# Performance work log

Measured on AMD Instinct MI355X. Metric: run time of the kernel, lower is better.

Reference implementation:

```python
import jax, jax.numpy as jnp
import numpy as np

C = 128
HEADS = 4
GROUPS = 16
EPS = 1e-5


def setup_inputs() -> dict:
    key = jax.random.key(0)
    ks = jax.random.split(key, 4)
    x = jax.random.normal(ks[0], (2, C, 16, 16, 16), dtype=jnp.float32)
    gn_w = jnp.ones((C,), dtype=jnp.float32)
    gn_b = jnp.zeros((C,), dtype=jnp.float32)
    w_qkv = jax.random.normal(ks[1], (3 * C, C), dtype=jnp.float32) * (1.0 / np.sqrt(C))
    w_out = jax.random.normal(ks[2], (C, C), dtype=jnp.float32) * (1.0 / np.sqrt(C))
    b_out = jnp.zeros((C,), dtype=jnp.float32)
    return {"x": x, "gn_w": gn_w, "gn_b": gn_b, "w_qkv": w_qkv, "w_out": w_out, "b_out": b_out}


def reference(x, gn_w, gn_b, w_qkv, w_out, b_out):
    b, c, d, h, w = x.shape
    L = d * h * w
    xf = x.reshape(b, c, L)  # flatten spatial dims -> tokens

    # GroupNorm over (channels-in-group, spatial)
    xg = xf.reshape(b, GROUPS, c // GROUPS * L)
    mean = jnp.mean(xg, axis=-1, keepdims=True)
    var = jnp.var(xg, axis=-1, keepdims=True)
    xn = ((xg - mean) * jax.lax.rsqrt(var + EPS)).reshape(b, c, L)
    xn = xn * gn_w[None, :, None] + gn_b[None, :, None]

    # 1x1 conv QKV projection (no bias)
    qkv = jnp.einsum('bcl,oc->bol', xn, w_qkv)  # (b, 3c, L)
    q, k, v = jnp.split(qkv, 3, axis=1)
    dh = c // HEADS
    q = q.reshape(b, HEADS, dh, L).transpose(0, 1, 3, 2)  # (b,H,L,dh)
    k = k.reshape(b, HEADS, dh, L)                        # (b,H,dh,L)
    v = v.reshape(b, HEADS, dh, L).transpose(0, 1, 3, 2)  # (b,H,L,dh)

    scale = dh ** (-0.5)
    attn = jnp.einsum('bhld,bhdm->bhlm', q, k) * scale    # (b,H,L,L)
    attn = jax.nn.softmax(attn, axis=-1)
    o = jnp.einsum('bhlm,bhmd->bhld', attn, v)            # (b,H,L,dh)
    o = o.transpose(0, 1, 3, 2).reshape(b, c, L)

    # output 1x1 conv with bias
    o = jnp.einsum('bcl,oc->bol', o, w_out) + b_out[None, :, None]
    return x + o.reshape(b, c, d, h, w)
```

## Files before the change

### kernel.cpp

```cpp
#include <hip/hip_runtime.h>
#include <math.h>

#define BB 2
#define CCH 128
#define LL 4096
#define HEADS 4
#define DH 32
#define EPSV 1e-5f
#define NSP 4

typedef float f32x4 __attribute__((ext_vector_type(4)));
typedef short bf16x8 __attribute__((ext_vector_type(8)));

__device__ inline unsigned short f2bf(float x) {
    union { float f; unsigned u; } v; v.f = x;
    unsigned r = v.u + 0x7fffu + ((v.u >> 16) & 1u);
    return (unsigned short)(r >> 16);
}
__device__ inline float bfbits2f(unsigned bits_hi16) {
    union { unsigned u; float f; } v; v.u = bits_hi16; return v.f;
}
__device__ inline float bfu(unsigned short s) {
    union { unsigned u; float f; } v; v.u = (unsigned)s << 16; return v.f;
}
__device__ inline unsigned cvtpk(float lo, float hi) {
    unsigned r;
    asm("v_cvt_pk_bf16_f32 %0, %1, %2" : "=v"(r) : "v"(lo), "v"(hi));
    return r;
}

__global__ __launch_bounds__(256) void gn_part(const float* __restrict__ x,
                                               float* __restrict__ ps, float* __restrict__ ps2) {
    const float* xp = x + (size_t)blockIdx.x * 4096;
    float s = 0.f, s2 = 0.f;
#pragma unroll
    for (int it = 0; it < 4; ++it) {
        float4 v = *(const float4*)(xp + it * 1024 + threadIdx.x * 4);
        s += v.x + v.y + v.z + v.w;
        s2 += v.x * v.x + v.y * v.y + v.z * v.z + v.w * v.w;
    }
    for (int off = 32; off; off >>= 1) {
        s += __shfl_down(s, off);
        s2 += __shfl_down(s2, off);
    }
    __shared__ float rs[4], rs2[4];
    int wave = threadIdx.x >> 6, lane = threadIdx.x & 63;
    if (lane == 0) { rs[wave] = s; rs2[wave] = s2; }
    __syncthreads();
    if (threadIdx.x == 0) {
        ps[blockIdx.x] = rs[0] + rs[1] + rs[2] + rs[3];
        ps2[blockIdx.x] = rs2[0] + rs2[1] + rs2[2] + rs2[3];
    }
}

__global__ void gn_final(const float* __restrict__ ps, const float* __restrict__ ps2,
                         float* __restrict__ sm, float* __restrict__ sr) {
    int t = threadIdx.x;
    if (t >= 32) return;
    float s = 0.f, s2 = 0.f;
#pragma unroll
    for (int i = 0; i < 8; ++i) { s += ps[t * 8 + i]; s2 += ps2[t * 8 + i]; }
    float mean = s / 32768.f;
    float var = s2 / 32768.f - mean * mean;
    sm[t] = mean;
    sr[t] = rsqrtf(var + EPSV);
}

__global__ __launch_bounds__(256) void prep_w(const float* __restrict__ w_qkv,
                                              const float* __restrict__ w_out,
                                              unsigned short* __restrict__ Wqh, unsigned short* __restrict__ Wql,
                                              unsigned short* __restrict__ Woh, unsigned short* __restrict__ Wol) {
    int i = blockIdx.x * 256 + threadIdx.x;
    const float qscale = 0.2550350f;
    if (i < 49152) {
        float v = w_qkv[i];
        if (i < 16384) v *= qscale;
        unsigned short h = f2bf(v);
        Wqh[i] = h;
        Wql[i] = f2bf(v - bfbits2f((unsigned)h << 16));
    } else {
        int j = i - 49152;
        float v = w_out[j];
        unsigned short h = f2bf(v);
        Woh[j] = h;
        Wol[j] = f2bf(v - bfbits2f((unsigned)h << 16));
    }
}

__global__ __launch_bounds__(256) void gn_apply_t(const float* __restrict__ x,
                                                  const float* __restrict__ gw, const float* __restrict__ gb,
                                                  const float* __restrict__ sm, const float* __restrict__ sr,
                                                  unsigned short* __restrict__ xth, unsigned short* __restrict__ xtl) {
    int lt = blockIdx.x, ct = blockIdx.y, b = blockIdx.z;
    int c0 = ct * 32, l0 = lt * 64;
    __shared__ float wsh[32], bsh[32], msh[4], rsh[4];
    __shared__ unsigned short sh[32][72], sl[32][72];
    if (threadIdx.x < 32) { wsh[threadIdx.x] = gw[c0 + threadIdx.x]; bsh[threadIdx.x] = gb[c0 + threadIdx.x]; }
    if (threadIdx.x < 4) {
        int g = (c0 >> 3) + threadIdx.x;
        msh[threadIdx.x] = sm[b * 16 + g];
        rsh[threadIdx.x] = sr[b * 16 + g];
    }
    __syncthreads();
#pragma unroll
    for (int it = 0; it < 2; ++it) {
        int idx = it * 256 + threadIdx.x;
        int cc = idx >> 4, l4 = idx & 15;
        float4 v = *(const float4*)(x + ((size_t)(b * CCH + c0 + cc)) * LL + l0 + l4 * 4);
        float mn = msh[cc >> 3], rstd = rsh[cc >> 3], w = wsh[cc], bv = bsh[cc];
        float a0 = (v.x - mn) * rstd * w + bv;
        float a1 = (v.y - mn) * rstd * w + bv;
        float a2 = (v.z - mn) * rstd * w + bv;
        float a3 = (v.w - mn) * rstd * w + bv;
        unsigned uh01 = cvtpk(a0, a1), uh23 = cvtpk(a2, a3);
        float r0 = a0 - bfbits2f(uh01 << 16), r1 = a1 - bfbits2f(uh01 & 0xffff0000u);
        float r2 = a2 - bfbits2f(uh23 << 16), r3 = a3 - bfbits2f(uh23 & 0xffff0000u);
        unsigned ul01 = cvtpk(r0, r1), ul23 = cvtpk(r2, r3);
        *(uint2*)&sh[cc][l4 * 4] = make_uint2(uh01, uh23);
        *(uint2*)&sl[cc][l4 * 4] = make_uint2(ul01, ul23);
    }
    __syncthreads();
    int l = threadIdx.x >> 2, c8 = threadIdx.x & 3;
    unsigned hw[4], lw[4];
#pragma unroll
    for (int j = 0; j < 4; ++j) {
        int c = c8 * 8 + 2 * j;
        hw[j] = (unsigned)sh[c][l] | ((unsigned)sh[c + 1][l] << 16);
        lw[j] = (unsigned)sl[c][l] | ((unsigned)sl[c + 1][l] << 16);
    }
    *(uint4*)(xth + ((size_t)b * LL + l0 + l) * CCH + c0 + c8 * 8) = make_uint4(hw[0], hw[1], hw[2], hw[3]);
    *(uint4*)(xtl + ((size_t)b * LL + l0 + l) * CCH + c0 + c8 * 8) = make_uint4(lw[0], lw[1], lw[2], lw[3]);
}

__global__ __launch_bounds__(64) void qkv_gemm(const unsigned short* __restrict__ xth,
                                               const unsigned short* __restrict__ xtl,
                                               const unsigned short* __restrict__ Wqh,
                                               const unsigned short* __restrict__ Wql,
                                               unsigned short* __restrict__ Qd,
                                               unsigned short* __restrict__ Kd,
                                               unsigned short* __restrict__ Vb) {
    int lt = blockIdx.x, og = blockIdx.y, b = blockIdx.z;
    int lane = threadIdx.x & 63, lm = lane & 15, lg = lane >> 4;
    int l0 = lt * 16;
    bf16x8 ah[4], al[4];
#pragma unroll
    for (int ks = 0; ks < 4; ++ks) {
        size_t off = ((size_t)b * LL + l0 + lm) * CCH + ks * 32 + 8 * lg;
        ah[ks] = *(const bf16x8*)(xth + off);
        al[ks] = *(const bf16x8*)(xtl + off);
    }
    f32x4 acc[8];
#pragma unroll
    for (int ot = 0; ot < 8; ++ot) acc[ot] = (f32x4){0.f, 0.f, 0.f, 0.f};
#pragma unroll
    for (int ot = 0; ot < 8; ++ot) {
#pragma unroll
        for (int ks = 0; ks < 4; ++ks) {
            size_t woff = (size_t)((og * 8 + ot) * 16 + lm) * CCH + ks * 32 + 8 * lg;
            bf16x8 wh = *(const bf16x8*)(Wqh + woff);
            bf16x8 wl = *(const bf16x8*)(Wql + woff);
            acc[ot] = __builtin_amdgcn_mfma_f32_16x16x32_bf16(ah[ks], wh, acc[ot], 0, 0, 0);
            acc[ot] = __builtin_amdgcn_mfma_f32_16x16x32_bf16(ah[ks], wl, acc[ot], 0, 0, 0);
            acc[ot] = __builtin_amdgcn_mfma_f32_16x16x32_bf16(al[ks], wh, acc[ot], 0, 0, 0);
        }
    }
    unsigned short* base = (og == 0) ? Qd : (og == 1) ? Kd : Vb;
#pragma unroll
    for (int ot = 0; ot < 8; ++ot) {
        int h = ot >> 1, d = (ot & 1) * 16 + lm;
        uint2 u;
        u.x = cvtpk(acc[ot][0], acc[ot][1]);
        u.y = cvtpk(acc[ot][2], acc[ot][3]);
        *(uint2*)(base + ((size_t)(b * HEADS + h) * DH + d) * LL + l0 + 4 * lg) = u;
    }
}

__global__ __launch_bounds__(256) void trQK(const unsigned short* __restrict__ Qd,
                                            const unsigned short* __restrict__ Kd,
                                            unsigned short* __restrict__ Qb,
                                            unsigned short* __restrict__ Kb) {
    int lt = blockIdx.x, bh = blockIdx.y, sel = blockIdx.z;
    const unsigned short* src = sel ? Kd : Qd;
    unsigned short* dst = sel ? Kb : Qb;
    int l0 = lt * 256;
    __shared__ unsigned short st[32][264];
#pragma unroll
    for (int it = 0; it < 4; ++it) {
        int idx = it * 256 + threadIdx.x;
        int d = idx >> 5, l8 = idx & 31;
        uint4 v = *(const uint4*)(src + ((size_t)bh * DH + d) * LL + l0 + l8 * 8);
        *(uint4*)&st[d][l8 * 8] = v;
    }
    __syncthreads();
    int t = threadIdx.x;
    unsigned w[16];
#pragma unroll
    for (int dp = 0; dp < 16; ++dp)
        w[dp] = (unsigned)st[2 * dp][t] | ((unsigned)st[2 * dp + 1][t] << 16);
    uint4* dp4 = (uint4*)(dst + ((size_t)bh * LL + l0 + t) * DH);
#pragma unroll
    for (int i = 0; i < 4; ++i)
        dp4[i] = make_uint4(w[4 * i], w[4 * i + 1], w[4 * i + 2], w[4 * i + 3]);
}

__global__ __launch_bounds__(256) void attn_kernel(const unsigned short* __restrict__ Qp,
                                                   const unsigned short* __restrict__ Kp,
                                                   const unsigned short* __restrict__ Vp,
                                                   unsigned short* __restrict__ AccB, float* __restrict__ Ls) {
    __shared__ __align__(16) unsigned short Ksh[2][64][40];
    __shared__ __align__(16) unsigned short Vsh[2][32][72];
    __shared__ __align__(16) short Pl[4][2][16][72];
    int id = blockIdx.x;
    int combo = id & 31, qb = id >> 5;
    int bh = combo >> 2, sp = combo & 3;
    int wid = threadIdx.x >> 6, lane = threadIdx.x & 63, lm = lane & 15, lg = lane >> 4;
    int q0 = qb * 128 + wid * 32;
    int kv0 = sp * 1024;
    int t = threadIdx.x;

    const unsigned short* Kbh = Kp + (size_t)bh * LL * DH;
    const unsigned short* Vbh = Vp + (size_t)bh * DH * LL;

    bf16x8 qf[2];
    qf[0] = *(const bf16x8*)(Qp + ((size_t)bh * LL + q0 + lm) * DH + 8 * lg);
    qf[1] = *(const bf16x8*)(Qp + ((size_t)bh * LL + q0 + 16 + lm) * DH + 8 * lg);

    f32x4 accO[2][2];
#pragma unroll
    for (int qi = 0; qi < 2; ++qi)
#pragma unroll
        for (int dt = 0; dt < 2; ++dt) accO[qi][dt] = (f32x4){0.f, 0.f, 0.f, 0.f};
    float plsum[2] = {0.f, 0.f};
    const f32x4 cbias = {-24.f, -24.f, -24.f, -24.f};

    int skv = t >> 2, ssl = (t & 3) * 8;
    int svd = t >> 3, svs = (t & 7) * 8;
    const uint4* gK = (const uint4*)(Kbh + (size_t)(kv0 + skv) * DH + ssl);
    const uint4* gV = (const uint4*)(Vbh + (size_t)svd * LL + kv0 + svs);
    uint4 kreg = *gK;
    uint4 vreg = *gV;

    for (int tt = 0; tt < 16; ++tt) {
        int cur = tt & 1;
        *(uint4*)&Ksh[cur][skv][ssl] = kreg;
        *(uint4*)&Vsh[cur][svd][svs] = vreg;
        if (tt < 15) { gK += 256; gV += 8; kreg = *gK; vreg = *gV; }
        __syncthreads();

        bf16x8 kf[4];
#pragma unroll
        for (int kc = 0; kc < 4; ++kc)
            kf[kc] = *(const bf16x8*)&Ksh[cur][kc * 16 + lm][lg * 8];
        f32x4 s[2][4];
#pragma unroll
        for (int qi = 0; qi < 2; ++qi)
#pragma unroll
            for (int kc = 0; kc < 4; ++kc)
                s[qi][kc] = __builtin_amdgcn_mfma_f32_16x16x32_bf16(kf[kc], qf[qi], cbias, 0, 0, 0);

        bf16x8 vf[2][2];
#pragma unroll
        for (int ch = 0; ch < 2; ++ch)
#pragma unroll
            for (int dt = 0; dt < 2; ++dt)
                vf[ch][dt] = *(const bf16x8*)&Vsh[cur][dt * 16 + lm][ch * 32 + 8 * lg];

#pragma unroll
        for (int qi = 0; qi < 2; ++qi) {
#pragma unroll
            for (int kc = 0; kc < 4; ++kc) {
                float e0 = __builtin_amdgcn_exp2f(s[qi][kc][0]);
                float e1 = __builtin_amdgcn_exp2f(s[qi][kc][1]);
                float e2 = __builtin_amdgcn_exp2f(s[qi][kc][2]);
                float e3 = __builtin_amdgcn_exp2f(s[qi][kc][3]);
                plsum[qi] += (e0 + e1) + (e2 + e3);
                uint2 u;
                u.x = cvtpk(e0, e1);
                u.y = cvtpk(e2, e3);
                *(uint2*)&Pl[wid][qi][lm][kc * 16 + 4 * lg] = u;
            }
            bf16x8 pf[2];
#pragma unroll
            for (int ch = 0; ch < 2; ++ch)
                pf[ch] = *(const bf16x8*)&Pl[wid][qi][lm][ch * 32 + 8 * lg];
#pragma unroll
            for (int ch = 0; ch < 2; ++ch)
#pragma unroll
                for (int dt = 0; dt < 2; ++dt)
                    accO[qi][dt] = __builtin_amdgcn_mfma_f32_16x16x32_bf16(vf[ch][dt], pf[ch], accO[qi][dt], 0, 0, 0);
        }
    }

#pragma unroll
    for (int qi = 0; qi < 2; ++qi) {
        float pl = plsum[qi];
        pl += __shfl_xor(pl, 16);
        pl += __shfl_xor(pl, 32);
#pragma unroll
        for (int dt = 0; dt < 2; ++dt) {
            uint2 u;
            u.x = cvtpk(accO[qi][dt][0], accO[qi][dt][1]);
            u.y = cvtpk(accO[qi][dt][2], accO[qi][dt][3]);
            *(uint2*)(AccB + ((size_t)(sp * 8 + bh) * LL + q0 + qi * 16 + lm) * DH + dt * 16 + 4 * lg) = u;
        }
        if (lg == 0) Ls[(size_t)(sp * 8 + bh) * LL + q0 + qi * 16 + lm] = pl;
    }
}

__global__ __launch_bounds__(256) void out_gemm(const unsigned short* __restrict__ AccB,
                                                const float* __restrict__ Ls,
                                                const unsigned short* __restrict__ Woh,
                                                const unsigned short* __restrict__ Wol,
                                                const float* __restrict__ bo,
                                                const float* __restrict__ x,
                                                float* __restrict__ out) {
    int lt = blockIdx.x, b = blockIdx.y;
    int wid = threadIdx.x >> 6, lane = threadIdx.x & 63, lm = lane & 15, lg = lane >> 4;
    int l0 = lt * 16;
    bf16x8 af[4];
#pragma unroll
    for (int ks = 0; ks < 4; ++ks) {
        int bh = b * HEADS + ks;
        float sum[8];
#pragma unroll
        for (int j = 0; j < 8; ++j) sum[j] = 0.f;
        float ls = 0.f;
#pragma unroll
        for (int sp = 0; sp < NSP; ++sp) {
            const unsigned short* ap = AccB + ((size_t)(sp * 8 + bh) * LL + l0 + lm) * DH + 8 * lg;
            uint4 v = *(const uint4*)ap;
            unsigned w0 = v.x, w1 = v.y, w2 = v.z, w3 = v.w;
            sum[0] += bfu((unsigned short)w0); sum[1] += bfu((unsigned short)(w0 >> 16));
            sum[2] += bfu((unsigned short)w1); sum[3] += bfu((unsigned short)(w1 >> 16));
            sum[4] += bfu((unsigned short)w2); sum[5] += bfu((unsigned short)(w2 >> 16));
            sum[6] += bfu((unsigned short)w3); sum[7] += bfu((unsigned short)(w3 >> 16));
            ls += Ls[(size_t)(sp * 8 + bh) * LL + l0 + lm];
        }
        float inv = 1.f / ls;
        union { unsigned u[4]; bf16x8 v; } cv;
        cv.u[0] = cvtpk(sum[0] * inv, sum[1] * inv);
        cv.u[1] = cvtpk(sum[2] * inv, sum[3] * inv);
        cv.u[2] = cvtpk(sum[4] * inv, sum[5] * inv);
        cv.u[3] = cvtpk(sum[6] * inv, sum[7] * inv);
        af[ks] = cv.v;
    }
    f32x4 acc[2];
    acc[0] = (f32x4){0.f, 0.f, 0.f, 0.f};
    acc[1] = (f32x4){0.f, 0.f, 0.f, 0.f};
#pragma unroll
    for (int oi = 0; oi < 2; ++oi) {
        int ot = wid * 2 + oi;
#pragma unroll
        for (int ks = 0; ks < 4; ++ks) {
            size_t woff = (size_t)(ot * 16 + lm) * CCH + ks * 32 + 8 * lg;
            bf16x8 wh = *(const bf16x8*)(Woh + woff);
            bf16x8 wl = *(const bf16x8*)(Wol + woff);
            acc[oi] = __builtin_amdgcn_mfma_f32_16x16x32_bf16(af[ks], wh, acc[oi], 0, 0, 0);
            acc[oi] = __builtin_amdgcn_mfma_f32_16x16x32_bf16(af[ks], wl, acc[oi], 0, 0, 0);
        }
    }
#pragma unroll
    for (int oi = 0; oi < 2; ++oi) {
        int oc = (wid * 2 + oi) * 16 + lm;
        float bias = bo[oc];
        size_t off = ((size_t)b * CCH + oc) * LL + l0 + 4 * lg;
        f32x4 xr = *(const f32x4*)(x + off);
        f32x4 r = acc[oi];
        r[0] += bias + xr[0];
        r[1] += bias + xr[1];
        r[2] += bias + xr[2];
        r[3] += bias + xr[3];
        *(f32x4*)(out + off) = r;
    }
}

extern "C" void kernel_launch(void* const* d_in, const int* in_sizes, int n_in,
                              void* d_out, int out_size, void* d_ws, size_t ws_size,
                              hipStream_t stream) {
    const float* x = (const float*)d_in[0];
    const float* gn_w = (const float*)d_in[1];
    const float* gn_b = (const float*)d_in[2];
    const float* w_qkv = (const float*)d_in[3];
    const float* w_out = (const float*)d_in[4];
    const float* b_out = (const float*)d_in[5];
    float* out = (float*)d_out;

    char* W = (char*)d_ws;
    unsigned short* xth = (unsigned short*)(W);
    unsigned short* xtl = (unsigned short*)(W + (2 << 20));
    unsigned short* Qd = (unsigned short*)(W + (4 << 20));
    unsigned short* Kd = (unsigned short*)(W + (6 << 20));
    unsigned short* Vb = (unsigned short*)(W + (8 << 20));
    unsigned short* Qb = (unsigned short*)(W + (10 << 20));
    unsigned short* Kb = (unsigned short*)(W + (12 << 20));
    unsigned short* AccB = (unsigned short*)(W);
    float* Ls = (float*)(W + (14 << 20));
    float* ps = (float*)(W + (14 << 20) + (600 << 10));
    float* ps2 = ps + 256;
    float* sm = ps2 + 256;
    float* sr = sm + 32;
    unsigned short* Wqh = (unsigned short*)(sr + 32);
    unsigned short* Wql = Wqh + 49152;
    unsigned short* Woh = Wql + 49152;
    unsigned short* Wol = Woh + 16384;

    gn_part<<<dim3(256), dim3(256), 0, stream>>>(x, ps, ps2);
    gn_final<<<dim3(1), dim3(64), 0, stream>>>(ps, ps2, sm, sr);
    prep_w<<<dim3(256), dim3(256), 0, stream>>>(w_qkv, w_out, Wqh, Wql, Woh, Wol);
    gn_apply_t<<<dim3(64, 4, BB), dim3(256), 0, stream>>>(x, gn_w, gn_b, sm, sr, xth, xtl);
    qkv_gemm<<<dim3(256, 3, BB), dim3(64), 0, stream>>>(xth, xtl, Wqh, Wql, Qd, Kd, Vb);
    trQK<<<dim3(16, BB * HEADS, 2), dim3(256), 0, stream>>>(Qd, Kd, Qb, Kb);
    attn_kernel<<<dim3(1024), dim3(256), 0, stream>>>(Qb, Kb, Vb, AccB, Ls);
    out_gemm<<<dim3(256, BB), dim3(256), 0, stream>>>(AccB, Ls, Woh, Wol, b_out, x, out);
}
```

Before: 91.73 us.

## Fuse GroupNorm finalize and weight prep, load attention K/V directly from global

Weight bf16 splitting is merged into the GroupNorm partial-sum kernel as extra blocks. The group statistics finalize step is folded into gn_apply_t, which removes two kernel launches. The attention kernel drops its shared-memory K/V staging and the per-tile __syncthreads: each wave now loads K fragments from global memory (prefetched one tile ahead) and V fragments directly. The P staging buffer is double-buffered in place of the barrier. This trades launch overhead and block-wide syncs for redundant per-wave global/L2 reads of K and V, and V reads that are strided across rows.

```diff
diff --git a/kernel.cpp b/kernel.cpp
--- a/kernel.cpp
+++ b/kernel.cpp
@@ -30,7 +30,29 @@
 }
 
 __global__ __launch_bounds__(256) void gn_part(const float* __restrict__ x,
-                                               float* __restrict__ ps, float* __restrict__ ps2) {
+                                               const float* __restrict__ w_qkv,
+                                               const float* __restrict__ w_out,
+                                               float* __restrict__ ps, float* __restrict__ ps2,
+                                               unsigned short* __restrict__ Wqh, unsigned short* __restrict__ Wql,
+                                               unsigned short* __restrict__ Woh, unsigned short* __restrict__ Wol) {
+    if (blockIdx.x >= 256) {
+        int i = (blockIdx.x - 256) * 256 + threadIdx.x;
+        const float qscale = 0.2550350f;
+        if (i < 49152) {
+            float v = w_qkv[i];
+            if (i < 16384) v *= qscale;
+            unsigned short h = f2bf(v);
+            Wqh[i] = h;
+            Wql[i] = f2bf(v - bfbits2f((unsigned)h << 16));
+        } else {
+            int j = i - 49152;
+            float v = w_out[j];
+            unsigned short h = f2bf(v);
+            Woh[j] = h;
+            Wol[j] = f2bf(v - bfbits2f((unsigned)h << 16));
+        }
+        return;
+    }
     const float* xp = x + (size_t)blockIdx.x * 4096;
     float s = 0.f, s2 = 0.f;
 #pragma unroll
@@ -53,43 +75,9 @@
     }
 }
 
-__global__ void gn_final(const float* __restrict__ ps, const float* __restrict__ ps2,
-                         float* __restrict__ sm, float* __restrict__ sr) {
-    int t = threadIdx.x;
-    if (t >= 32) return;
-    float s = 0.f, s2 = 0.f;
-#pragma unroll
-    for (int i = 0; i < 8; ++i) { s += ps[t * 8 + i]; s2 += ps2[t * 8 + i]; }
-    float mean = s / 32768.f;
-    float var = s2 / 32768.f - mean * mean;
-    sm[t] = mean;
-    sr[t] = rsqrtf(var + EPSV);
-}
-
-__global__ __launch_bounds__(256) void prep_w(const float* __restrict__ w_qkv,
-                                              const float* __restrict__ w_out,
-                                              unsigned short* __restrict__ Wqh, unsigned short* __restrict__ Wql,
-                                              unsigned short* __restrict__ Woh, unsigned short* __restrict__ Wol) {
-    int i = blockIdx.x * 256 + threadIdx.x;
-    const float qscale = 0.2550350f;
-    if (i < 49152) {
-        float v = w_qkv[i];
-        if (i < 16384) v *= qscale;
-        unsigned short h = f2bf(v);
-        Wqh[i] = h;
-        Wql[i] = f2bf(v - bfbits2f((unsigned)h << 16));
-    } else {
-        int j = i - 49152;
-        float v = w_out[j];
-        unsigned short h = f2bf(v);
-        Woh[j] = h;
-        Wol[j] = f2bf(v - bfbits2f((unsigned)h << 16));
-    }
-}
-
 __global__ __launch_bounds__(256) void gn_apply_t(const float* __restrict__ x,
                                                   const float* __restrict__ gw, const float* __restrict__ gb,
-                                                  const float* __restrict__ sm, const float* __restrict__ sr,
+                                                  const float* __restrict__ ps, const float* __restrict__ ps2,
                                                   unsigned short* __restrict__ xth, unsigned short* __restrict__ xtl) {
     int lt = blockIdx.x, ct = blockIdx.y, b = blockIdx.z;
     int c0 = ct * 32, l0 = lt * 64;
@@ -97,9 +85,17 @@
     __shared__ unsigned short sh[32][72], sl[32][72];
     if (threadIdx.x < 32) { wsh[threadIdx.x] = gw[c0 + threadIdx.x]; bsh[threadIdx.x] = gb[c0 + threadIdx.x]; }
     if (threadIdx.x < 4) {
-        int g = (c0 >> 3) + threadIdx.x;
-        msh[threadIdx.x] = sm[b * 16 + g];
-        rsh[threadIdx.x] = sr[b * 16 + g];
+        int g = ct * 4 + threadIdx.x;
+        float s = 0.f, s2 = 0.f;
+#pragma unroll
+        for (int i = 0; i < 8; ++i) {
+            s += ps[b * CCH + g * 8 + i];
+            s2 += ps2[b * CCH + g * 8 + i];
+        }
+        float mean = s / 32768.f;
+        float var = s2 / 32768.f - mean * mean;
+        msh[threadIdx.x] = mean;
+        rsh[threadIdx.x] = rsqrtf(var + EPSV);
     }
     __syncthreads();
 #pragma unroll
@@ -207,16 +203,13 @@
                                                    const unsigned short* __restrict__ Kp,
                                                    const unsigned short* __restrict__ Vp,
                                                    unsigned short* __restrict__ AccB, float* __restrict__ Ls) {
-    __shared__ __align__(16) unsigned short Ksh[2][64][40];
-    __shared__ __align__(16) unsigned short Vsh[2][32][72];
-    __shared__ __align__(16) short Pl[4][2][16][72];
+    __shared__ __align__(16) short Pl[2][4][2][16][72];
     int id = blockIdx.x;
     int combo = id & 31, qb = id >> 5;
     int bh = combo >> 2, sp = combo & 3;
     int wid = threadIdx.x >> 6, lane = threadIdx.x & 63, lm = lane & 15, lg = lane >> 4;
     int q0 = qb * 128 + wid * 32;
     int kv0 = sp * 1024;
-    int t = threadIdx.x;
 
     const unsigned short* Kbh = Kp + (size_t)bh * LL * DH;
     const unsigned short* Vbh = Vp + (size_t)bh * DH * LL;
@@ -233,24 +226,20 @@
     float plsum[2] = {0.f, 0.f};
     const f32x4 cbias = {-24.f, -24.f, -24.f, -24.f};
 
-    int skv = t >> 2, ssl = (t & 3) * 8;
-    int svd = t >> 3, svs = (t & 7) * 8;
-    const uint4* gK = (const uint4*)(Kbh + (size_t)(kv0 + skv) * DH + ssl);
-    const uint4* gV = (const uint4*)(Vbh + (size_t)svd * LL + kv0 + svs);
-    uint4 kreg = *gK;
-    uint4 vreg = *gV;
+    bf16x8 kf[4];
+#pragma unroll
+    for (int kc = 0; kc < 4; ++kc)
+        kf[kc] = *(const bf16x8*)(Kbh + ((size_t)(kv0 + kc * 16 + lm)) * DH + 8 * lg);
 
     for (int tt = 0; tt < 16; ++tt) {
         int cur = tt & 1;
-        *(uint4*)&Ksh[cur][skv][ssl] = kreg;
-        *(uint4*)&Vsh[cur][svd][svs] = vreg;
-        if (tt < 15) { gK += 256; gV += 8; kreg = *gK; vreg = *gV; }
-        __syncthreads();
-
-        bf16x8 kf[4];
+        int m0 = kv0 + tt * 64;
+        int mn = kv0 + (((tt + 1) & 15) << 6);
+        bf16x8 kn[4];
 #pragma unroll
         for (int kc = 0; kc < 4; ++kc)
-            kf[kc] = *(const bf16x8*)&Ksh[cur][kc * 16 + lm][lg * 8];
+            kn[kc] = *(const bf16x8*)(Kbh + ((size_t)(mn + kc * 16 + lm)) * DH + 8 * lg);
+
         f32x4 s[2][4];
 #pragma unroll
         for (int qi = 0; qi < 2; ++qi)
@@ -263,7 +252,7 @@
         for (int ch = 0; ch < 2; ++ch)
 #pragma unroll
             for (int dt = 0; dt < 2; ++dt)
-                vf[ch][dt] = *(const bf16x8*)&Vsh[cur][dt * 16 + lm][ch * 32 + 8 * lg];
+                vf[ch][dt] = *(const bf16x8*)(Vbh + ((size_t)(dt * 16 + lm)) * LL + m0 + ch * 32 + 8 * lg);
 
 #pragma unroll
         for (int qi = 0; qi < 2; ++qi) {
@@ -277,18 +266,22 @@
                 uint2 u;
                 u.x = cvtpk(e0, e1);
                 u.y = cvtpk(e2, e3);
-                *(uint2*)&Pl[wid][qi][lm][kc * 16 + 4 * lg] = u;
+                *(uint2*)&Pl[cur][wid][qi][lm][kc * 16 + 4 * lg] = u;
             }
             bf16x8 pf[2];
 #pragma unroll
             for (int ch = 0; ch < 2; ++ch)
-                pf[ch] = *(const bf16x8*)&Pl[wid][qi][lm][ch * 32 + 8 * lg];
+                pf[ch] = *(const bf16x8*)&Pl[cur][wid][qi][lm][ch * 32 + 8 * lg];
+            asm volatile("" ::: "memory");
 #pragma unroll
             for (int ch = 0; ch < 2; ++ch)
 #pragma unroll
                 for (int dt = 0; dt < 2; ++dt)
                     accO[qi][dt] = __builtin_amdgcn_mfma_f32_16x16x32_bf16(vf[ch][dt], pf[ch], accO[qi][dt], 0, 0, 0);
         }
+
+#pragma unroll
+        for (int kc = 0; kc < 4; ++kc) kf[kc] = kn[kc];
     }
 
 #pragma unroll
@@ -397,17 +390,13 @@
     float* Ls = (float*)(W + (14 << 20));
     float* ps = (float*)(W + (14 << 20) + (600 << 10));
     float* ps2 = ps + 256;
-    float* sm = ps2 + 256;
-    float* sr = sm + 32;
-    unsigned short* Wqh = (unsigned short*)(sr + 32);
+    unsigned short* Wqh = (unsigned short*)(ps2 + 256);
     unsigned short* Wql = Wqh + 49152;
     unsigned short* Woh = Wql + 49152;
     unsigned short* Wol = Woh + 16384;
 
-    gn_part<<<dim3(256), dim3(256), 0, stream>>>(x, ps, ps2);
-    gn_final<<<dim3(1), dim3(64), 0, stream>>>(ps, ps2, sm, sr);
-    prep_w<<<dim3(256), dim3(256), 0, stream>>>(w_qkv, w_out, Wqh, Wql, Woh, Wol);
-    gn_apply_t<<<dim3(64, 4, BB), dim3(256), 0, stream>>>(x, gn_w, gn_b, sm, sr, xth, xtl);
+    gn_part<<<dim3(512), dim3(256), 0, stream>>>(x, w_qkv, w_out, ps, ps2, Wqh, Wql, Woh, Wol);
+    gn_apply_t<<<dim3(64, 4, BB), dim3(256), 0, stream>>>(x, gn_w, gn_b, ps, ps2, xth, xtl);
     qkv_gemm<<<dim3(256, 3, BB), dim3(64), 0, stream>>>(xth, xtl, Wqh, Wql, Qd, Kd, Vb);
     trQK<<<dim3(16, BB * HEADS, 2), dim3(256), 0, stream>>>(Qd, Kd, Qb, Kb);
     attn_kernel<<<dim3(1024), dim3(256), 0, stream>>>(Qb, Kb, Vb, AccB, Ls);
```

After: 112.2 us. 22.3% more time.
